# Performance work log

Measured on AMD Instinct MI355X. Metric: run time of the kernel, lower is better.

Reference implementation:

```python
import jax, jax.numpy as jnp
import numpy as np

MOD_EMBED_DIM = 16
HIDDEN = 64
NUM_MODALITIES = 3
MLP_IN = 2 + 2 * MOD_EMBED_DIM + 2  # 36


def setup_inputs() -> dict:
    key = jax.random.key(0)
    ks = jax.random.split(key, 4)
    h, w = 40, 40
    return {
        "h": h,
        "w": w,
        "q_mod": 0,
        "k_mod": 2,
        "structure_map": jax.random.normal(ks[0], (4, 1, 80, 80), jnp.float32),
        "mod_embed": jax.random.normal(ks[1], (NUM_MODALITIES, MOD_EMBED_DIM), jnp.float32),
        "W1": jax.random.normal(ks[2], (MLP_IN, HIDDEN), jnp.float32) * 0.1,
        "b1": jnp.zeros((HIDDEN,), jnp.float32),
        "W2": jax.random.normal(ks[3], (HIDDEN, 1), jnp.float32) * 0.1,
        "b2": jnp.zeros((1,), jnp.float32),
    }


def reference(h, w, q_mod, k_mod, structure_map, mod_embed, W1, b1, W2, b2):
    # --- coords on a [-0.5, 0.5] grid, flattened row-major -> (N, 2) as (x, y)
    ys = jnp.linspace(-0.5, 0.5, h)
    xs = jnp.linspace(-0.5, 0.5, w)
    yy, xx = jnp.meshgrid(ys, xs, indexing="ij")
    coords = jnp.stack([xx, yy], axis=-1).reshape(-1, 2)  # (N, 2)
    N = coords.shape[0]

    # relative coords per pair (i, j): (N, N, 2)
    rel = coords[:, None, :] - coords[None, :, :]

    # modality pair embedding: constant across all pairs -> (2*E,)
    mod_vec = jnp.concatenate([mod_embed[q_mod], mod_embed[k_mod]])

    # structure: bilinear resize to (h, w) (half-pixel == align_corners=False),
    # then mean over batch -> per-position scalar s_mean: (N,)
    b = structure_map.shape[0]
    s = jax.image.resize(structure_map, (b, 1, h, w), method="linear")
    s_mean = s.reshape(-1, 1, N)[:, 0, :].mean(axis=0)  # (N,)

    # First linear layer applied to the (implicit) concat
    # [rel, mod_vec, s_i, s_j] by splitting W1 — same math as concat @ W1,
    # but avoids materializing the (N^2, 36) concat tensor.
    W_rel = W1[:2]            # (2, H)
    W_mod = W1[2:2 + 2 * MOD_EMBED_DIM]  # (32, H)
    W_si = W1[-2]             # (H,)
    W_sj = W1[-1]             # (H,)

    hid = (
        jnp.einsum("ijc,ch->ijh", rel, W_rel)
        + (mod_vec @ W_mod + b1)
        + s_mean[:, None, None] * W_si
        + s_mean[None, :, None] * W_sj
    )  # (N, N, H)
    hid = jax.nn.relu(hid)
    bias = jnp.einsum("ijh,ho->ijo", hid, W2) + b2  # (N, N, 1)
    return bias.reshape(1, 1, N, N)
```

## Files before the change

kernel.cpp:

```cpp
#include <hip/hip_runtime.h>

#define HIN  80
#define WIN  80
#define NB   4
#define HOUT 40
#define WOUT 40
#define NPTS (HOUT*WOUT)
#define NHID 64

__global__ __launch_bounds__(256) void rpe_fused(
    const int* __restrict__ qmod, const int* __restrict__ kmod,
    const float* __restrict__ smap, const float* __restrict__ mode,
    const float* __restrict__ W1, const float* __restrict__ b1,
    const float* __restrict__ W2, const float* __restrict__ b2,
    float* __restrict__ out)
{
    __shared__ float As[64][68];
    __shared__ float Cs[64][68];
    __shared__ float w0s[NHID], w1s[NHID], wis[NHID], wjs[NHID], bases[NHID];
    __shared__ float sxi[64], syi[64], smi[64];
    __shared__ float sxj[64], syj[64], smj[64];
    __shared__ float linA[64], linC[64];

    const int t  = threadIdx.x;
    const int bi = blockIdx.y, bj = blockIdx.x;

    if (t < 64) {
        const int q = qmod[0], k = kmod[0];
        w0s[t] = W1[t];
        w1s[t] = W1[NHID + t];
        wis[t] = W1[34*NHID + t];
        wjs[t] = W1[35*NHID + t];
        float bacc = b1[t];
        #pragma unroll
        for (int m = 0; m < 16; ++m) bacc = fmaf(mode[q*16 + m], W1[(2 + m)*NHID + t], bacc);
        #pragma unroll
        for (int m = 0; m < 16; ++m) bacc = fmaf(mode[k*16 + m], W1[(18 + m)*NHID + t], bacc);
        bases[t] = bacc;
    } else if (t < 192) {
        const int isJ = (t >= 128) ? 1 : 0;
        const int idx = t - (isJ ? 128 : 64);
        const int p   = (isJ ? bj : bi) * 64 + idx;
        const int oy = p / WOUT, ox = p % WOUT;
        float wy[4], wx[4]; int iy[4], ix[4];
        float wsy = 0.f, wsx = 0.f;
        #pragma unroll
        for (int d = 0; d < 4; ++d) {
            const float wv = (d == 0 || d == 3) ? 0.25f : 0.75f;
            const int yi = 2*oy + d - 1;
            const int xi = 2*ox + d - 1;
            iy[d] = yi < 0 ? 0 : (yi >= HIN ? HIN - 1 : yi);
            ix[d] = xi < 0 ? 0 : (xi >= WIN ? WIN - 1 : xi);
            wy[d] = (yi >= 0 && yi < HIN) ? wv : 0.f;
            wx[d] = (xi >= 0 && xi < WIN) ? wv : 0.f;
            wsy += wy[d]; wsx += wx[d];
        }
        float acc = 0.f;
        #pragma unroll
        for (int b = 0; b < NB; ++b) {
            const float* bp = smap + b*HIN*WIN;
            #pragma unroll
            for (int dy = 0; dy < 4; ++dy) {
                const float* rp = bp + iy[dy]*WIN;
                float rs = 0.f;
                #pragma unroll
                for (int dx = 0; dx < 4; ++dx) rs = fmaf(wx[dx], rp[ix[dx]], rs);
                acc = fmaf(wy[dy], rs, acc);
            }
        }
        const float sm = acc / (wsy * wsx * (float)NB);
        const float x = -0.5f + (float)ox * (1.0f/(float)(WOUT-1));
        const float y = -0.5f + (float)oy * (1.0f/(float)(HOUT-1));
        if (isJ) { sxj[idx] = x; syj[idx] = y; smj[idx] = sm; }
        else     { sxi[idx] = x; syi[idx] = y; smi[idx] = sm; }
    }
    __syncthreads();

    {
        const int h = t & 63;
        const int g = t >> 6;
        const float w0 = w0s[h], w1v = w1s[h], wiv = wis[h], wjv = wjs[h], bb = bases[h];
        #pragma unroll
        for (int r = 0; r < 16; ++r) {
            const int row = g*16 + r;
            As[row][h] = fmaf(sxi[row], w0, fmaf(syi[row], w1v, fmaf(smi[row], wiv, bb)));
            Cs[row][h] = fmaf(smj[row], wjv, -fmaf(sxj[row], w0, syj[row] * w1v));
        }
    }
    __syncthreads();

    if (t < 128) {
        const int p = t & 63;
        const float* row = (t < 64) ? &As[p][0] : &Cs[p][0];
        float s = 0.f;
        #pragma unroll
        for (int h = 0; h < NHID; h += 4) {
            const float4 r4 = *(const float4*)(row + h);
            s = fmaf(r4.x, 0.5f*W2[h+0],
                fmaf(r4.y, 0.5f*W2[h+1],
                fmaf(r4.z, 0.5f*W2[h+2],
                fmaf(r4.w, 0.5f*W2[h+3], s))));
        }
        if (t < 64) linA[p] = s; else linC[p] = s;
    }

    const int tx = t & 15;
    const int ty = t >> 4;

    float4 acc[4][4];
    #pragma unroll
    for (int ii = 0; ii < 4; ++ii)
        #pragma unroll
        for (int jj = 0; jj < 4; ++jj) acc[ii][jj] = make_float4(0.f, 0.f, 0.f, 0.f);

    #pragma unroll
    for (int h = 0; h < NHID; h += 4) {
        const float w2x = 0.5f*W2[h+0], w2y = 0.5f*W2[h+1];
        const float w2z = 0.5f*W2[h+2], w2w = 0.5f*W2[h+3];
        float4 a[4], c[4];
        #pragma unroll
        for (int ii = 0; ii < 4; ++ii) a[ii] = *(const float4*)&As[ty + ii*16][h];
        #pragma unroll
        for (int jj = 0; jj < 4; ++jj) c[jj] = *(const float4*)&Cs[tx + jj*16][h];
        #pragma unroll
        for (int ii = 0; ii < 4; ++ii) {
            #pragma unroll
            for (int jj = 0; jj < 4; ++jj) {
                acc[ii][jj].x = fmaf(fabsf(a[ii].x + c[jj].x), w2x, acc[ii][jj].x);
                acc[ii][jj].y = fmaf(fabsf(a[ii].y + c[jj].y), w2y, acc[ii][jj].y);
                acc[ii][jj].z = fmaf(fabsf(a[ii].z + c[jj].z), w2z, acc[ii][jj].z);
                acc[ii][jj].w = fmaf(fabsf(a[ii].w + c[jj].w), w2w, acc[ii][jj].w);
            }
        }
    }

    __syncthreads();

    const float bias2 = b2[0];
    float la[4], lc[4];
    #pragma unroll
    for (int ii = 0; ii < 4; ++ii) la[ii] = linA[ty + ii*16];
    #pragma unroll
    for (int jj = 0; jj < 4; ++jj) lc[jj] = linC[tx + jj*16];

    #pragma unroll
    for (int ii = 0; ii < 4; ++ii) {
        const int i = bi*64 + ty + ii*16;
        float* orow = out + (size_t)i*NPTS + bj*64;
        #pragma unroll
        for (int jj = 0; jj < 4; ++jj) {
            const float4 a4 = acc[ii][jj];
            orow[tx + jj*16] = ((a4.x + a4.y) + (a4.z + a4.w))
                             + (la[ii] + lc[jj]) + bias2;
        }
    }
}

extern "C" void kernel_launch(void* const* d_in, const int* in_sizes, int n_in,
                              void* d_out, int out_size, void* d_ws, size_t ws_size,
                              hipStream_t stream) {
    const int*   qm   = (const int*)d_in[2];
    const int*   km   = (const int*)d_in[3];
    const float* smap = (const float*)d_in[4];
    const float* mode = (const float*)d_in[5];
    const float* W1   = (const float*)d_in[6];
    const float* b1   = (const float*)d_in[7];
    const float* W2   = (const float*)d_in[8];
    const float* b2   = (const float*)d_in[9];
    float* out = (float*)d_out;
    (void)d_ws; (void)ws_size;

    rpe_fused<<<dim3(NPTS/64, NPTS/64), 256, 0, stream>>>(
        qm, km, smap, mode, W1, b1, W2, b2, out);
}
```

Baseline: 86.44 us.

## Store hidden pre-activations in fp16 and use packed add plus fdot2 accumulation

Converts the per-row A and per-column C hidden pre-activation tiles to half precision in LDS. The inner loop now does packed fp16 adds, clears sign bits with a mask to take the absolute value, and accumulates with v_dot2 into fp32, replacing scalar fp32 add/abs/fma. This halves LDS traffic and roughly halves the ALU instruction count of the hot loop. The cost is reduced precision of the hidden values and of W2, which may exceed tolerance.

```diff
diff --git a/kernel.cpp b/kernel.cpp
--- a/kernel.cpp
+++ b/kernel.cpp
@@ -1,4 +1,5 @@
 #include <hip/hip_runtime.h>
+#include <string.h>
 
 #define HIN  80
 #define WIN  80
@@ -8,6 +9,21 @@
 #define NPTS (HOUT*WOUT)
 #define NHID 64
 
+typedef _Float16 h2 __attribute__((ext_vector_type(2)));
+typedef _Float16 h8 __attribute__((ext_vector_type(8)));
+typedef unsigned int u4 __attribute__((ext_vector_type(4)));
+
+union h8u { h8 v; h2 p[4]; u4 u; };
+
+
+__device__ __forceinline__ float dot2acc(h2 a, h2 b, float c) {
+#if __has_builtin(__builtin_amdgcn_fdot2)
+    return __builtin_amdgcn_fdot2(a, b, c, false);
+#else
+    return c + (float)a.x * (float)b.x + (float)a.y * (float)b.y;
+#endif
+}
+
 __global__ __launch_bounds__(256) void rpe_fused(
     const int* __restrict__ qmod, const int* __restrict__ kmod,
     const float* __restrict__ smap, const float* __restrict__ mode,
@@ -15,8 +31,9 @@
     const float* __restrict__ W2, const float* __restrict__ b2,
     float* __restrict__ out)
 {
-    __shared__ float As[64][68];
-    __shared__ float Cs[64][68];
+    __shared__ __attribute__((aligned(16))) _Float16 Ash[64][72];
+    __shared__ __attribute__((aligned(16))) _Float16 Csh[64][72];
+    __shared__ __attribute__((aligned(16))) _Float16 w2h[NHID];
     __shared__ float w0s[NHID], w1s[NHID], wis[NHID], wjs[NHID], bases[NHID];
     __shared__ float sxi[64], syi[64], smi[64];
     __shared__ float sxj[64], syj[64], smj[64];
@@ -31,6 +48,7 @@
         w1s[t] = W1[NHID + t];
         wis[t] = W1[34*NHID + t];
         wjs[t] = W1[35*NHID + t];
+        w2h[t] = (_Float16)(0.5f * W2[t]);
         float bacc = b1[t];
         #pragma unroll
         for (int m = 0; m < 16; ++m) bacc = fmaf(mode[q*16 + m], W1[(2 + m)*NHID + t], bacc);
@@ -83,23 +101,25 @@
         #pragma unroll
         for (int r = 0; r < 16; ++r) {
             const int row = g*16 + r;
-            As[row][h] = fmaf(sxi[row], w0, fmaf(syi[row], w1v, fmaf(smi[row], wiv, bb)));
-            Cs[row][h] = fmaf(smj[row], wjv, -fmaf(sxj[row], w0, syj[row] * w1v));
+            const float av = fmaf(sxi[row], w0, fmaf(syi[row], w1v, fmaf(smi[row], wiv, bb)));
+            const float cv = fmaf(smj[row], wjv, -fmaf(sxj[row], w0, syj[row] * w1v));
+            Ash[row][h] = (_Float16)av;
+            Csh[row][h] = (_Float16)cv;
         }
     }
     __syncthreads();
 
     if (t < 128) {
         const int p = t & 63;
-        const float* row = (t < 64) ? &As[p][0] : &Cs[p][0];
+        const _Float16* row = (t < 64) ? &Ash[p][0] : &Csh[p][0];
         float s = 0.f;
         #pragma unroll
-        for (int h = 0; h < NHID; h += 4) {
-            const float4 r4 = *(const float4*)(row + h);
-            s = fmaf(r4.x, 0.5f*W2[h+0],
-                fmaf(r4.y, 0.5f*W2[h+1],
-                fmaf(r4.z, 0.5f*W2[h+2],
-                fmaf(r4.w, 0.5f*W2[h+3], s))));
+        for (int o = 0; o < 8; ++o) {
+            h8u r8, w8;
+            r8.v = *(const h8*)(row + o*8);
+            w8.v = *(const h8*)(&w2h[o*8]);
+            #pragma unroll
+            for (int k = 0; k < 4; ++k) s = dot2acc(r8.p[k], w8.p[k], s);
         }
         if (t < 64) linA[p] = s; else linC[p] = s;
     }
@@ -114,22 +134,25 @@
         for (int jj = 0; jj < 4; ++jj) acc[ii][jj] = make_float4(0.f, 0.f, 0.f, 0.f);
 
     #pragma unroll
-    for (int h = 0; h < NHID; h += 4) {
-        const float w2x = 0.5f*W2[h+0], w2y = 0.5f*W2[h+1];
-        const float w2z = 0.5f*W2[h+2], w2w = 0.5f*W2[h+3];
-        float4 a[4], c[4];
+    for (int o = 0; o < 8; ++o) {
+        const int h = o*8;
+        h8u w8; w8.v = *(const h8*)(&w2h[h]);
+        h8 a8[4], c8[4];
         #pragma unroll
-        for (int ii = 0; ii < 4; ++ii) a[ii] = *(const float4*)&As[ty + ii*16][h];
+        for (int ii = 0; ii < 4; ++ii) a8[ii] = *(const h8*)(&Ash[ty + ii*16][h]);
         #pragma unroll
-        for (int jj = 0; jj < 4; ++jj) c[jj] = *(const float4*)&Cs[tx + jj*16][h];
+        for (int jj = 0; jj < 4; ++jj) c8[jj] = *(const h8*)(&Csh[tx + jj*16][h]);
         #pragma unroll
         for (int ii = 0; ii < 4; ++ii) {
             #pragma unroll
             for (int jj = 0; jj < 4; ++jj) {
-                acc[ii][jj].x = fmaf(fabsf(a[ii].x + c[jj].x), w2x, acc[ii][jj].x);
-                acc[ii][jj].y = fmaf(fabsf(a[ii].y + c[jj].y), w2y, acc[ii][jj].y);
-                acc[ii][jj].z = fmaf(fabsf(a[ii].z + c[jj].z), w2z, acc[ii][jj].z);
-                acc[ii][jj].w = fmaf(fabsf(a[ii].w + c[jj].w), w2w, acc[ii][jj].w);
+                h8u t8;
+                t8.v = a8[ii] + c8[jj];
+                t8.u &= 0x7FFF7FFFu;
+                acc[ii][jj].x = dot2acc(t8.p[0], w8.p[0], acc[ii][jj].x);
+                acc[ii][jj].y = dot2acc(t8.p[1], w8.p[1], acc[ii][jj].y);
+                acc[ii][jj].z = dot2acc(t8.p[2], w8.p[2], acc[ii][jj].z);
+                acc[ii][jj].w = dot2acc(t8.p[3], w8.p[3], acc[ii][jj].w);
             }
         }
     }
```

Measured after the change: 87.06 us. No clear change (+0.7%).
